# Optimization experiments

Hardware: AMD Instinct MI355X
Metric: run time of the kernel (lower is better)

## Reference

```python
import jax, jax.numpy as jnp
import numpy as np

# Lorentz hyperboloid with curvature -1 (k = 1): <x,x>_L = -1/k, x0 = time coord.
K_CURV = 1.0
EPS = 1e-8
B, N, D, H = 4, 1024, 1024, 16
HD = D // H  # dim_per_head = 64 (space dims per head)


def _time(space):
    # time coord so the point lies on the hyperboloid
    return jnp.sqrt(jnp.sum(space * space, axis=-1, keepdims=True) + 1.0 / K_CURV)


def _lift(space):
    return jnp.concatenate([_time(space), space], axis=-1)


def _linner(u, v):
    # Minkowski inner product <u,v>_L = -u0 v0 + u_s . v_s
    return jnp.sum(u[..., 1:] * v[..., 1:], axis=-1) - u[..., 0] * v[..., 0]


def _lorentz_layernorm(x, gamma, beta):
    s = x[..., 1:]
    mu = jnp.mean(s, axis=-1, keepdims=True)
    var = jnp.mean((s - mu) ** 2, axis=-1, keepdims=True)
    s = (s - mu) / jnp.sqrt(var + 1e-5) * gamma + beta
    return _lift(s)


def _lorentz_linear(x, W, b):
    # linear on the full Lorentz point -> space part of output, time recomputed
    return _lift(x @ W + b)


def _lresnet(x, y, w):
    # Lorentzian residual: (x + w*y) renormalized back onto the hyperboloid
    z = x + w * y
    denom = jnp.sqrt(jnp.clip(-_linner(z, z), EPS))[..., None]
    return z / (jnp.sqrt(K_CURV) * denom)


def _attention(x, Wq, bq, Wk, bk, Wv, bv, Wo, bo):
    def heads(W, b):
        s = (x @ W + b).reshape(B, N, H, HD).transpose(0, 2, 1, 3)  # [B,H,N,HD]
        return _lift(s)  # per-head Lorentz points [B,H,N,HD+1]

    q, k, v = heads(Wq, bq), heads(Wk, bk), heads(Wv, bv)
    sgn = jnp.concatenate([-jnp.ones((1,), x.dtype), jnp.ones((HD,), x.dtype)])
    # pairwise Minkowski inner products; score = -d_L^2 = 2/k + 2<q,k>_L, scaled
    scores = jnp.einsum('bhqd,bhkd->bhqk', q * sgn, k)
    scores = (2.0 / K_CURV + 2.0 * scores) / np.sqrt(HD).astype(np.float32)
    attn = jax.nn.softmax(scores, axis=-1)
    # Lorentz midpoint aggregation of values
    mid = jnp.einsum('bhqk,bhkd->bhqd', attn, v)
    denom = jnp.sqrt(jnp.clip(-_linner(mid, mid), EPS))[..., None]
    mid = mid / (jnp.sqrt(K_CURV) * denom)  # [B,H,N,HD+1]
    cat = mid.transpose(0, 2, 1, 3).reshape(B, N, H * (HD + 1))  # trans_heads_concat
    return _lift(cat @ Wo + bo)


def reference(x, g1, b1, Wq, bq, Wk, bk, Wv, bv, Wo, bo, g2, b2, Wfc, bfc, Wpj, bpj, w1, w2):
    lx = _lorentz_layernorm(x, g1, b1)
    ax = _attention(lx, Wq, bq, Wk, bk, Wv, bv, Wo, bo)
    x = _lresnet(x, ax, w1)
    h = _lorentz_layernorm(x, g2, b2)
    h = _lorentz_linear(h, Wfc, bfc)                      # [B,N,4D]
    h = _lift(jax.nn.gelu(h[..., 1:], approximate=False))  # LorentzActivation(GELU)
    h = _lorentz_linear(h, Wpj, bpj)                      # [B,N,D]
    return _lresnet(x, h, w2)


def setup_inputs() -> dict:
    key = jax.random.key(0)
    ks = jax.random.split(key, 8)
    sc = 0.02
    f32 = jnp.float32
    xs = jax.random.normal(ks[0], (B, N, D - 1), f32)
    return dict(
        x=_lift(xs),
        g1=jnp.ones((D - 1,), f32), b1=jnp.zeros((D - 1,), f32),
        Wq=sc * jax.random.normal(ks[1], (D, H * HD), f32), bq=jnp.zeros((H * HD,), f32),
        Wk=sc * jax.random.normal(ks[2], (D, H * HD), f32), bk=jnp.zeros((H * HD,), f32),
        Wv=sc * jax.random.normal(ks[3], (D, H * HD), f32), bv=jnp.zeros((H * HD,), f32),
        Wo=sc * jax.random.normal(ks[4], (H * (HD + 1), D - 1), f32), bo=jnp.zeros((D - 1,), f32),
        g2=jnp.ones((D - 1,), f32), b2=jnp.zeros((D - 1,), f32),
        Wfc=sc * jax.random.normal(ks[5], (D, 4 * D - 1), f32), bfc=jnp.zeros((4 * D - 1,), f32),
        Wpj=sc * jax.random.normal(ks[6], (4 * D, D - 1), f32), bpj=jnp.zeros((D - 1,), f32),
        w1=jnp.ones((), f32), w2=jnp.ones((), f32),
    )
```

## Files before the change

kernel.cpp:

```cpp
#include <hip/hip_runtime.h>
#include <math.h>

#define BB 4
#define NN 1024
#define DD 1024
#define HH 16
#define ROWS (BB*NN)

typedef __attribute__((ext_vector_type(8))) short bf16x8;
typedef __attribute__((ext_vector_type(4))) float f32x4;
typedef __attribute__((ext_vector_type(4))) unsigned short u16x4;
typedef __attribute__((ext_vector_type(8))) unsigned short u16x8;
typedef unsigned short u16;

__device__ __forceinline__ u16 f2bf(float f) {
    union { float f; unsigned u; } v; v.f = f;
    unsigned r = v.u + 0x7fff + ((v.u >> 16) & 1);
    return (u16)(r >> 16);
}
__device__ __forceinline__ float bf2f(u16 u) {
    union { unsigned u; float f; } v; v.u = ((unsigned)u) << 16; return v.f;
}

__device__ __forceinline__ void async16(const void* g, void* l) {
    __builtin_amdgcn_global_load_lds(
        (__attribute__((address_space(1))) void*)(uintptr_t)g,
        (__attribute__((address_space(3))) void*)(uintptr_t)l,
        16, 0, 0);
}

__device__ __forceinline__ float block_reduce_sum(float v, float* sm) {
    #pragma unroll
    for (int o = 32; o > 0; o >>= 1) v += __shfl_down(v, o);
    int lane = threadIdx.x & 63, wid = threadIdx.x >> 6;
    if (lane == 0) sm[wid] = v;
    __syncthreads();
    if (wid == 0) {
        v = (lane < (int)(blockDim.x >> 6)) ? sm[lane] : 0.f;
        #pragma unroll
        for (int o = 2; o > 0; o >>= 1) v += __shfl_down(v, o);
        if (lane == 0) sm[0] = v;
    }
    __syncthreads();
    float r = sm[0];
    __syncthreads();
    return r;
}

__device__ __forceinline__ void block_reduce3(float& a, float& b, float& c, float* sm) {
    #pragma unroll
    for (int o = 32; o > 0; o >>= 1) {
        a += __shfl_down(a, o); b += __shfl_down(b, o); c += __shfl_down(c, o);
    }
    int lane = threadIdx.x & 63, wid = threadIdx.x >> 6;
    if (lane == 0) { sm[wid] = a; sm[8 + wid] = b; sm[16 + wid] = c; }
    __syncthreads();
    int nw = (int)(blockDim.x >> 6);
    if (wid == 0) {
        float va = (lane < nw) ? sm[lane] : 0.f;
        float vb = (lane < nw) ? sm[8 + lane] : 0.f;
        float vc = (lane < nw) ? sm[16 + lane] : 0.f;
        #pragma unroll
        for (int o = 2; o > 0; o >>= 1) {
            va += __shfl_down(va, o); vb += __shfl_down(vb, o); vc += __shfl_down(vc, o);
        }
        if (lane == 0) { sm[0] = va; sm[8] = vb; sm[16] = vc; }
    }
    __syncthreads();
    a = sm[0]; b = sm[8]; c = sm[16];
    __syncthreads();
}

__global__ __launch_bounds__(256) void k_pre(
        const float* __restrict__ Wq_, const float* __restrict__ Wk_,
        const float* __restrict__ Wv_, const float* __restrict__ Wo_,
        const float* __restrict__ Wfc_, const float* __restrict__ Wpj_,
        u16* __restrict__ WqkvT, u16* __restrict__ WoT,
        u16* __restrict__ WfcT, u16* __restrict__ WpjT,
        const float* __restrict__ x, const float* __restrict__ g1,
        const float* __restrict__ be1, u16* __restrict__ lnout) {
    __shared__ float t[32][33];
    int bid = blockIdx.x;
    if (bid < 12352) {
        const float* W; u16* out; int K, N, Kpad, Npad, gx;
        if (bid < 1024)      { W = Wq_;  out = WqkvT;            K = 1024; N = 1024; Kpad = 1024; Npad = 1024; gx = 32; }
        else if (bid < 2048) { W = Wk_;  out = WqkvT + 1048576;  K = 1024; N = 1024; Kpad = 1024; Npad = 1024; gx = 32; bid -= 1024; }
        else if (bid < 3072) { W = Wv_;  out = WqkvT + 2097152;  K = 1024; N = 1024; Kpad = 1024; Npad = 1024; gx = 32; bid -= 2048; }
        else if (bid < 4160) { W = Wo_;  out = WoT;              K = 1040; N = 1023; Kpad = 1088; Npad = 1024; gx = 34; bid -= 3072; }
        else if (bid < 8256) { W = Wfc_; out = WfcT;             K = 1024; N = 4095; Kpad = 1024; Npad = 4096; gx = 32; bid -= 4160; }
        else                 { W = Wpj_; out = WpjT;             K = 4096; N = 1023; Kpad = 4096; Npad = 1024; gx = 128; bid -= 8256; }
        int k0 = (bid % gx) * 32, n0 = (bid / gx) * 32;
        int tx = threadIdx.x & 31, ty = threadIdx.x >> 5;
        #pragma unroll
        for (int i = 0; i < 32; i += 8) {
            int k = k0 + ty + i, n = n0 + tx;
            t[ty + i][tx] = (k < K && n < N) ? W[(size_t)k * N + n] : 0.f;
        }
        __syncthreads();
        #pragma unroll
        for (int i = 0; i < 32; i += 8) {
            int n = n0 + ty + i, k = k0 + tx;
            if (n < Npad && k < Kpad) out[(size_t)n * Kpad + k] = f2bf(t[tx][ty + i]);
        }
    } else {
        float* sm = &t[0][0];
        int row = bid - 12352, tid = threadIdx.x;
        const float4* xr4 = (const float4*)(x + (size_t)row * DD);
        float4 xv = xr4[tid];
        float s = 0.f, ss = 0.f, dummy = 0.f;
        #pragma unroll
        for (int e = 0; e < 4; ++e) {
            if (tid | e) {
                float v = ((const float*)&xv)[e];
                s += v; ss += v * v;
            }
        }
        block_reduce3(s, ss, dummy, sm);
        float mu = s * (1.f / 1023.f);
        float var = ss * (1.f / 1023.f) - mu * mu;
        float rstd = rsqrtf(var + 1e-5f);
        float vo[4]; float s2 = 0.f;
        #pragma unroll
        for (int e = 0; e < 4; ++e) {
            int c = 4 * tid + e;
            if (c > 0) {
                float v = (((const float*)&xv)[e] - mu) * rstd * g1[c - 1] + be1[c - 1];
                vo[e] = v; s2 += v * v;
            } else vo[e] = 0.f;
        }
        s2 = block_reduce_sum(s2, sm);
        u16x4 lo;
        #pragma unroll
        for (int e = 0; e < 4; ++e) lo[e] = f2bf(vo[e]);
        if (tid == 0) lo[0] = f2bf(sqrtf(s2 + 1.f));
        ((u16x4*)(lnout + (size_t)row * DD))[tid] = lo;
    }
}

__device__ __forceinline__ void cstore(float* p, float v) { *p = v; }
__device__ __forceinline__ void cstore(u16* p, float v) { *p = f2bf(v); }

template <typename OT>
__global__ __launch_bounds__(256) void k_gemm_mfma(
        const u16* __restrict__ A, const u16* __restrict__ BT,
        const float* __restrict__ bias, int nbias,
        OT* __restrict__ C0, OT* __restrict__ C1,
        int ldc, int ldab, int ksplit, int K, int swz) {
    __shared__ __align__(16) u16 smem[32768];
    int z = blockIdx.z;
    int kbeg = z ? ksplit : 0;
    int kend = z ? K : ksplit;
    OT* C = z ? C1 : C0;
    const float* bs = z ? nullptr : bias;

    int bx = blockIdx.x, by = blockIdx.y;
    if (swz) {
        int nx = gridDim.x, ny = gridDim.y;
        int flat = bx + nx * by;
        int c = flat & 7, i = flat >> 3;
        int hi = i / nx;
        by = c * (ny >> 3) + hi;
        bx = i - hi * nx;
    }

    int tid = threadIdx.x;
    int wave = tid >> 6, lane = tid & 63;
    int quad = lane >> 4, m16 = lane & 15;
    int n0 = bx * 128, m0 = by * 128;
    int wm = (wave & 1) * 64, wn = (wave >> 1) * 64;

    f32x4 acc[4][4];
    #pragma unroll
    for (int t = 0; t < 4; ++t)
        #pragma unroll
        for (int u = 0; u < 4; ++u) acc[t][u] = (f32x4){0.f, 0.f, 0.f, 0.f};

    int r8 = lane >> 3;
    int cc = (lane & 7) ^ r8;
    int srow = wave * 32 + r8;
    const u16* ag = A  + (size_t)(m0 + srow) * ldab + cc * 8;
    const u16* bg = BT + (size_t)(n0 + srow) * ldab + cc * 8;

    auto stage = [&](int k0, int s) {
        #pragma unroll
        for (int j = 0; j < 4; ++j) {
            async16(ag + (size_t)(j * 8) * ldab + k0, &smem[s * 8192 + (wave * 32 + j * 8) * 64]);
            async16(bg + (size_t)(j * 8) * ldab + k0, &smem[16384 + s * 8192 + (wave * 32 + j * 8) * 64]);
        }
    };

    int niter = (kend - kbeg) >> 6;
    stage(kbeg, 0);
    for (int it = 0; it < niter; ++it) {
        int cur = it & 1;
        __syncthreads();
        if (it + 1 < niter) stage(kbeg + (it + 1) * 64, cur ^ 1);
        #pragma unroll
        for (int kk = 0; kk < 2; ++kk) {
            bf16x8 af[4], bfr[4];
            #pragma unroll
            for (int t = 0; t < 4; ++t) {
                int slot = (kk * 4 + quad) ^ (m16 & 7);
                af[t] = *(const bf16x8*)&smem[cur * 8192 + (wm + t * 16 + m16) * 64 + slot * 8];
            }
            #pragma unroll
            for (int u = 0; u < 4; ++u) {
                int slot = (kk * 4 + quad) ^ (m16 & 7);
                bfr[u] = *(const bf16x8*)&smem[16384 + cur * 8192 + (wn + u * 16 + m16) * 64 + slot * 8];
            }
            #pragma unroll
            for (int t = 0; t < 4; ++t)
                #pragma unroll
                for (int u = 0; u < 4; ++u)
                    acc[t][u] = __builtin_amdgcn_mfma_f32_16x16x32_bf16(af[t], bfr[u], acc[t][u], 0, 0, 0);
        }
    }
    if constexpr (sizeof(OT) == 2) {
        __syncthreads();
        #pragma unroll
        for (int u = 0; u < 4; ++u) {
            int col = n0 + wn + u * 16 + m16;
            float bv = (bs != nullptr && col < nbias) ? bs[col] : 0.f;
            #pragma unroll
            for (int t = 0; t < 4; ++t) {
                #pragma unroll
                for (int r = 0; r < 4; ++r)
                    smem[(wm + t * 16 + quad * 4 + r) * 128 + wn + u * 16 + m16] = f2bf(acc[t][u][r] + bv);
            }
        }
        __syncthreads();
        u16* Cg = (u16*)C;
        for (int i = tid; i < 2048; i += 256) {
            int rr = i >> 4, ch = i & 15;
            ((u16x8*)(Cg + (size_t)(m0 + rr) * ldc + n0))[ch] = ((const u16x8*)(smem + rr * 128))[ch];
        }
    } else {
        #pragma unroll
        for (int u = 0; u < 4; ++u) {
            int col = n0 + wn + u * 16 + m16;
            if (col < nbias) {
                float bv = (bs != nullptr) ? bs[col] : 0.f;
                #pragma unroll
                for (int t = 0; t < 4; ++t) {
                    #pragma unroll
                    for (int r = 0; r < 4; ++r) {
                        int row = m0 + wm + t * 16 + quad * 4 + r;
                        cstore(C + (size_t)row * ldc + col, acc[t][u][r] + bv);
                    }
                }
            }
        }
    }
}

__global__ __launch_bounds__(256) void k_gemm_qkv(
        const u16* __restrict__ A, const u16* __restrict__ BT,
        const float* __restrict__ bq, const float* __restrict__ bk,
        const float* __restrict__ bv,
        u16* __restrict__ Qp, u16* __restrict__ Kp, u16* __restrict__ V2) {
    __shared__ __align__(16) u16 smem[32768];
    int tid = threadIdx.x;
    int wave = tid >> 6, lane = tid & 63;
    int quad = lane >> 4, m16 = lane & 15;
    int n0 = blockIdx.x * 128, m0 = blockIdx.y * 128;
    int wm = (wave & 1) * 64, wn = (wave >> 1) * 64;

    f32x4 acc[4][4];
    #pragma unroll
    for (int t = 0; t < 4; ++t)
        #pragma unroll
        for (int u = 0; u < 4; ++u) acc[t][u] = (f32x4){0.f, 0.f, 0.f, 0.f};

    int r8 = lane >> 3;
    int cc = (lane & 7) ^ r8;
    int srow = wave * 32 + r8;
    const u16* ag = A  + (size_t)(m0 + srow) * 1024 + cc * 8;
    const u16* bg = BT + (size_t)(n0 + srow) * 1024 + cc * 8;

    auto stage = [&](int k0, int s) {
        #pragma unroll
        for (int j = 0; j < 4; ++j) {
            async16(ag + (size_t)(j * 8) * 1024 + k0, &smem[s * 8192 + (wave * 32 + j * 8) * 64]);
            async16(bg + (size_t)(j * 8) * 1024 + k0, &smem[16384 + s * 8192 + (wave * 32 + j * 8) * 64]);
        }
    };

    stage(0, 0);
    for (int it = 0; it < 16; ++it) {
        int cur = it & 1;
        __syncthreads();
        if (it + 1 < 16) stage((it + 1) * 64, cur ^ 1);
        #pragma unroll
        for (int kk = 0; kk < 2; ++kk) {
            bf16x8 af[4], bfr[4];
            #pragma unroll
            for (int t = 0; t < 4; ++t) {
                int slot = (kk * 4 + quad) ^ (m16 & 7);
                af[t] = *(const bf16x8*)&smem[cur * 8192 + (wm + t * 16 + m16) * 64 + slot * 8];
            }
            #pragma unroll
            for (int u = 0; u < 4; ++u) {
                int slot = (kk * 4 + quad) ^ (m16 & 7);
                bfr[u] = *(const bf16x8*)&smem[16384 + cur * 8192 + (wn + u * 16 + m16) * 64 + slot * 8];
            }
            #pragma unroll
            for (int t = 0; t < 4; ++t)
                #pragma unroll
                for (int u = 0; u < 4; ++u)
                    acc[t][u] = __builtin_amdgcn_mfma_f32_16x16x32_bf16(af[t], bfr[u], acc[t][u], 0, 0, 0);
        }
    }

    int sec = n0 >> 10;
    int h = ((n0 & 1023) + wn) >> 6;
    int b = m0 >> 10;
    int b16h = b * 16 + h;
    const float* bias = (sec == 0) ? bq : (sec == 1) ? bk : bv;
    float bvu[4];
    #pragma unroll
    for (int u = 0; u < 4; ++u) bvu[u] = bias[h * 64 + u * 16 + m16];

    if (sec < 2) {
        const int strd = (sec == 0) ? 96 : 104;
        u16* P = (sec == 0) ? Qp : Kp;
        const float tsign = (sec == 0) ? -1.f : 1.f;
        #pragma unroll
        for (int t = 0; t < 4; ++t) {
            #pragma unroll
            for (int r = 0; r < 4; ++r) {
                int n = (m0 + wm + t * 16 + quad * 4 + r) & 1023;
                u16* drow = P + ((size_t)b16h * 1024 + n) * strd;
                float vv[4]; float ss = 0.f;
                #pragma unroll
                for (int u = 0; u < 4; ++u) { vv[u] = acc[t][u][r] + bvu[u]; ss += vv[u] * vv[u]; }
                ss += __shfl_xor(ss, 1); ss += __shfl_xor(ss, 2);
                ss += __shfl_xor(ss, 4); ss += __shfl_xor(ss, 8);
                #pragma unroll
                for (int u = 0; u < 4; ++u) drow[1 + u * 16 + m16] = f2bf(vv[u]);
                if (m16 == 0) drow[0] = f2bf(tsign * sqrtf(ss + 1.f));
                drow[65 + m16] = 0;
                if (m16 < 15) drow[81 + m16] = 0;
            }
        }
    } else {
        int tile = ((m0 & 1023) + wm) >> 6;
        size_t tbase = ((size_t)b16h * 16 + tile) * 6144;
        #pragma unroll
        for (int t = 0; t < 4; ++t) {
            int tok0 = t * 16 + quad * 4;
            u16x4 tc;
            u16x4 pk[4];
            #pragma unroll
            for (int r = 0; r < 4; ++r) {
                float vv[4]; float ss = 0.f;
                #pragma unroll
                for (int u = 0; u < 4; ++u) { vv[u] = acc[t][u][r] + bvu[u]; ss += vv[u] * vv[u]; }
                ss += __shfl_xor(ss, 1); ss += __shfl_xor(ss, 2);
                ss += __shfl_xor(ss, 4); ss += __shfl_xor(ss, 8);
                tc[r] = f2bf(sqrtf(ss + 1.f));
                #pragma unroll
                for (int u = 0; u < 4; ++u) pk[u][r] = f2bf(vv[u]);
            }
            #pragma unroll
            for (int u = 0; u < 4; ++u) {
                int d = u * 16 + m16;
                *(u16x4*)&V2[tbase + (size_t)(1 + d) * 72 + tok0] = pk[u];
            }
            if (m16 == 0) *(u16x4*)&V2[tbase + tok0] = tc;
        }
        for (int i = lane; i < 240; i += 64) {
            int rr = 65 + (i >> 4), sg = (i & 15) << 2;
            *(u16x4*)&V2[tbase + (size_t)rr * 72 + sg] = (u16x4){0, 0, 0, 0};
        }
    }
}

#define AKS 104
#define AVS 72
#define APS 88
#define KTILE_U16 (64 * AKS)
#define VTILE_U16 6144
#define EXPC 0.36067376f
__global__ __launch_bounds__(512) void k_attn_mfma(
        const u16* __restrict__ Qp, const u16* __restrict__ Kp,
        const u16* __restrict__ V2, u16* __restrict__ cat) {
    __shared__ __align__(16) u16 Klds[2][KTILE_U16];
    __shared__ __align__(16) u16 Vlds[2][VTILE_U16];
    __shared__ __align__(16) u16 Plds[8][16 * APS];
    int tid = threadIdx.x;
    int wave = tid >> 6, lane = tid & 63;
    int quad = lane >> 4, m = lane & 15;
    int wq = wave & 3, g = wave >> 2;
    int bid = blockIdx.x;
    int bh = ((bid & 7) << 3) | (bid >> 6);
    int qt = (bid >> 3) & 7;

    const u16* kg = Kp + (size_t)bh * 16 * KTILE_U16;
    const u16* vg = V2 + (size_t)bh * 16 * VTILE_U16;

    bf16x8 aq[3];
    {
        const u16* qptr = Qp + ((size_t)bh * 1024 + qt * 128 + g * 64 + wq * 16 + m) * 96;
        aq[0] = *(const bf16x8*)(qptr + quad * 8);
        aq[1] = *(const bf16x8*)(qptr + 32 + quad * 8);
        aq[2] = *(const bf16x8*)(qptr + 64 + quad * 8);
    }

    f32x4 O[5];
    #pragma unroll
    for (int i = 0; i < 5; ++i) O[i] = (f32x4){0.f, 0.f, 0.f, 0.f};

    auto stage = [&](int kt, int s) {
        const u16* kt_p = kg + kt * KTILE_U16 + lane * 8;
        const u16* vt_p = vg + kt * VTILE_U16 + lane * 8;
        for (int i = wave; i < 25; i += 8) {
            if (i < 13) async16(kt_p + i * 512, &Klds[s][i * 512]);
            else        async16(vt_p + (i - 13) * 512, &Vlds[s][(i - 13) * 512]);
        }
    };

    stage(0, 0);
    for (int kt = 0; kt < 16; ++kt) {
        int cur = kt & 1;
        __syncthreads();
        if (kt < 15) stage(kt + 1, cur ^ 1);
        u16* pw = &Plds[wave][0];
        #pragma unroll
        for (int nt = 0; nt < 4; ++nt) {
            f32x4 acc = (f32x4){0.f, 0.f, 0.f, 0.f};
            const u16* kr = &Klds[cur][(nt * 16 + m) * AKS + quad * 8];
            acc = __builtin_amdgcn_mfma_f32_16x16x32_bf16(*(const bf16x8*)(kr),      aq[0], acc, 0, 0, 0);
            acc = __builtin_amdgcn_mfma_f32_16x16x32_bf16(*(const bf16x8*)(kr + 32), aq[1], acc, 0, 0, 0);
            acc = __builtin_amdgcn_mfma_f32_16x16x32_bf16(*(const bf16x8*)(kr + 64), aq[2], acc, 0, 0, 0);
            unsigned pk0, pk1;
            {
                union { float f; unsigned u; } a0, a1, a2, a3;
                a0.f = __builtin_amdgcn_exp2f(fmaf(acc[0], EXPC, EXPC));
                a1.f = __builtin_amdgcn_exp2f(fmaf(acc[1], EXPC, EXPC));
                a2.f = __builtin_amdgcn_exp2f(fmaf(acc[2], EXPC, EXPC));
                a3.f = __builtin_amdgcn_exp2f(fmaf(acc[3], EXPC, EXPC));
                pk0 = ((a0.u + 0x8000u) >> 16) | (((a1.u + 0x8000u) >> 16) << 16);
                pk1 = ((a2.u + 0x8000u) >> 16) | (((a3.u + 0x8000u) >> 16) << 16);
            }
            uint2 pk; pk.x = pk0; pk.y = pk1;
            *(uint2*)&pw[m * APS + nt * 16 + quad * 4] = pk;
        }
        #pragma unroll
        for (int kc = 0; kc < 2; ++kc) {
            bf16x8 ap = *(const bf16x8*)&Plds[wave][m * APS + kc * 32 + quad * 8];
            #pragma unroll
            for (int vt = 0; vt < 5; ++vt) {
                bf16x8 bv = *(const bf16x8*)&Vlds[cur][(vt * 16 + m) * AVS + kc * 32 + quad * 8];
                O[vt] = __builtin_amdgcn_mfma_f32_16x16x32_bf16(ap, bv, O[vt], 0, 0, 0);
            }
        }
    }
    int b = bh >> 4, h = bh & 15;
    #pragma unroll
    for (int r = 0; r < 4; ++r) {
        float part = 0.f;
        #pragma unroll
        for (int vt = 0; vt < 5; ++vt) {
            int c = vt * 16 + m;
            float o = O[vt][r];
            part += (c == 0) ? o * o : -o * o;
        }
        part += __shfl_xor(part, 1);
        part += __shfl_xor(part, 2);
        part += __shfl_xor(part, 4);
        part += __shfl_xor(part, 8);
        float rden = rsqrtf(fmaxf(part, 1e-8f));
        int n = qt * 128 + g * 64 + wq * 16 + quad * 4 + r;
        u16* crow = cat + (size_t)(b * 1024 + n) * 1088 + h * 65;
        #pragma unroll
        for (int vt = 0; vt < 5; ++vt) {
            int c = vt * 16 + m;
            if (c < 65) crow[c] = f2bf(O[vt][r] * rden);
        }
    }
    if (h == 15) {
        for (int i = tid; i < 128 * 48; i += 512) {
            int rr = i / 48, c = i - rr * 48;
            int n = qt * 128 + rr;
            cat[(size_t)(b * 1024 + n) * 1088 + 1040 + c] = 0;
        }
    }
}

__global__ __launch_bounds__(256) void k_lresnet_ln(
        const float* __restrict__ x, const float* __restrict__ y0,
        const float* __restrict__ y1, const float* __restrict__ wscale,
        const float* __restrict__ g2, const float* __restrict__ be2,
        float* __restrict__ x1, u16* __restrict__ lnout) {
    __shared__ float sm[24];
    __shared__ float edge[256];
    int row = blockIdx.x, tid = threadIdx.x;
    float w = *wscale;
    float4 xv = ((const float4*)(x  + (size_t)row * DD))[tid];
    float4 av = ((const float4*)(y0 + (size_t)row * 1024))[tid];
    float4 bv = ((const float4*)(y1 + (size_t)row * 1024))[tid];
    float yv[4];
    #pragma unroll
    for (int e = 0; e < 4; ++e) yv[e] = ((const float*)&av)[e] + ((const float*)&bv)[e];
    edge[tid] = yv[3];
    float sy = 0.f;
    #pragma unroll
    for (int e = 0; e < 4; ++e) if (4 * tid + e < 1023) sy += yv[e] * yv[e];
    __syncthreads();
    float yprev = tid ? edge[tid - 1] : 0.f;
    float zv[4];
    float sz = 0.f, szs = 0.f;
    #pragma unroll
    for (int e = 0; e < 4; ++e) {
        float yc = (e == 0) ? yprev : yv[e - 1];
        float z = ((const float*)&xv)[e] + w * yc;
        zv[e] = z;
        if (tid | e) { sz += z * z; szs += z; }
    }
    block_reduce3(sy, sz, szs, sm);
    float x0 = x[(size_t)row * DD];
    float z0 = x0 + w * sqrtf(sy + 1.f);
    float q = z0 * z0 - sz;
    float rden = rsqrtf(fmaxf(q, 1e-8f));
    float mu = rden * szs * (1.f / 1023.f);
    float ex2 = rden * rden * sz * (1.f / 1023.f);
    float rstd = rsqrtf(ex2 - mu * mu + 1e-5f);
    float4 xo; float vo[4]; float s2 = 0.f;
    #pragma unroll
    for (int e = 0; e < 4; ++e) {
        int c = 4 * tid + e;
        float xn = zv[e] * rden;
        ((float*)&xo)[e] = xn;
        if (c > 0) {
            float v = (xn - mu) * rstd * g2[c - 1] + be2[c - 1];
            vo[e] = v; s2 += v * v;
        } else vo[e] = 0.f;
    }
    if (tid == 0) ((float*)&xo)[0] = z0 * rden;
    ((float4*)(x1 + (size_t)row * DD))[tid] = xo;
    s2 = block_reduce_sum(s2, sm);
    u16x4 lo;
    #pragma unroll
    for (int e = 0; e < 4; ++e) lo[e] = f2bf(vo[e]);
    if (tid == 0) lo[0] = f2bf(sqrtf(s2 + 1.f));
    ((u16x4*)(lnout + (size_t)row * DD))[tid] = lo;
}

__global__ __launch_bounds__(256) void k_lresnet(
        const float* __restrict__ x, const float* __restrict__ y0,
        const float* __restrict__ y1, const float* __restrict__ wscale,
        float* __restrict__ out) {
    __shared__ float sm[24];
    __shared__ float edge[256];
    int row = blockIdx.x, tid = threadIdx.x;
    float w = *wscale;
    float4 xv = ((const float4*)(x  + (size_t)row * DD))[tid];
    float4 av = ((const float4*)(y0 + (size_t)row * 1024))[tid];
    float4 bv = ((const float4*)(y1 + (size_t)row * 1024))[tid];
    float yv[4];
    #pragma unroll
    for (int e = 0; e < 4; ++e) yv[e] = ((const float*)&av)[e] + ((const float*)&bv)[e];
    edge[tid] = yv[3];
    float sy = 0.f;
    #pragma unroll
    for (int e = 0; e < 4; ++e) if (4 * tid + e < 1023) sy += yv[e] * yv[e];
    __syncthreads();
    float yprev = tid ? edge[tid - 1] : 0.f;
    float zv[4];
    float sz = 0.f, dummy = 0.f;
    #pragma unroll
    for (int e = 0; e < 4; ++e) {
        float yc = (e == 0) ? yprev : yv[e - 1];
        float z = ((const float*)&xv)[e] + w * yc;
        zv[e] = z;
        if (tid | e) sz += z * z;
    }
    block_reduce3(sy, sz, dummy, sm);
    float x0 = x[(size_t)row * DD];
    float z0 = x0 + w * sqrtf(sy + 1.f);
    float q = z0 * z0 - sz;
    float rden = rsqrtf(fmaxf(q, 1e-8f));
    float4 o;
    #pragma unroll
    for (int e = 0; e < 4; ++e) ((float*)&o)[e] = zv[e] * rden;
    if (tid == 0) ((float*)&o)[0] = z0 * rden;
    ((float4*)(out + (size_t)row * DD))[tid] = o;
}

__global__ __launch_bounds__(256) void k_gelu_lift(
        const u16* __restrict__ hfc, u16* __restrict__ hg) {
    __shared__ float sm[8];
    __shared__ u16 edge[512];
    int row = blockIdx.x, tid = threadIdx.x;
    const u16* hr = hfc + (size_t)row * 4096;
    u16* gr = hg + (size_t)row * 4096;
    u16x8 hv0 = *(const u16x8*)(hr + tid * 8);
    u16x8 hv1 = *(const u16x8*)(hr + 2048 + tid * 8);
    edge[tid] = hv0[7];
    edge[256 + tid] = hv1[7];
    __syncthreads();
    u16 p0 = tid ? edge[tid - 1] : (u16)0;
    u16 p1 = edge[255 + tid];
    float s2 = 0.f;
    u16x8 ov0, ov1;
    #pragma unroll
    for (int e = 0; e < 8; ++e) {
        int c = 8 * tid + e;
        float gl = 0.f;
        if (c > 0) {
            float v = bf2f((e == 0) ? p0 : hv0[e - 1]);
            gl = 0.5f * v * (1.f + erff(v * 0.70710678f));
            s2 += gl * gl;
        }
        ov0[e] = f2bf(gl);
    }
    #pragma unroll
    for (int e = 0; e < 8; ++e) {
        float v = bf2f((e == 0) ? p1 : hv1[e - 1]);
        float gl = 0.5f * v * (1.f + erff(v * 0.70710678f));
        s2 += gl * gl;
        ov1[e] = f2bf(gl);
    }
    *(u16x8*)(gr + tid * 8) = ov0;
    *(u16x8*)(gr + 2048 + tid * 8) = ov1;
    s2 = block_reduce_sum(s2, sm);
    if (tid == 0) gr[0] = f2bf(sqrtf(s2 + 1.f));
}

extern "C" void kernel_launch(void* const* d_in, const int* in_sizes, int n_in,
                              void* d_out, int out_size, void* d_ws, size_t ws_size,
                              hipStream_t stream) {
    const float* x   = (const float*)d_in[0];
    const float* g1  = (const float*)d_in[1];
    const float* b1  = (const float*)d_in[2];
    const float* Wq  = (const float*)d_in[3];
    const float* bq  = (const float*)d_in[4];
    const float* Wk  = (const float*)d_in[5];
    const float* bk  = (const float*)d_in[6];
    const float* Wv  = (const float*)d_in[7];
    const float* bv  = (const float*)d_in[8];
    const float* Wo  = (const float*)d_in[9];
    const float* bo  = (const float*)d_in[10];
    const float* g2  = (const float*)d_in[11];
    const float* b2  = (const float*)d_in[12];
    const float* Wfc = (const float*)d_in[13];
    const float* bfc = (const float*)d_in[14];
    const float* Wpj = (const float*)d_in[15];
    const float* bpj = (const float*)d_in[16];
    const float* w1  = (const float*)d_in[17];
    const float* w2  = (const float*)d_in[18];
    float* out = (float*)d_out;

    char* W = (char*)d_ws;
    u16* lx_bf  = (u16*)(W + 0);
    u16* WqkvT  = (u16*)(W + 8388608);
    u16* WoT    = (u16*)(W + 14680064);
    u16* WfcT   = (u16*)(W + 16908288);
    u16* WpjT   = (u16*)(W + 25296896);
    u16* Qp     = (u16*)(W + 58851328);
    u16* Kp     = (u16*)(W + 71434240);
    u16* V2     = (u16*)(W + 85065728);
    u16* cat_bf = (u16*)(W + 97648640);
    float* ax0  = (float*)(W + 33685504);
    float* ax1  = (float*)(W + 50462720);
    float* x1   = (float*)(W + 67239936);
    u16* hfc_bf = (u16*)(W + 84017152);
    u16* hg_bf  = (u16*)(W + 33685504);
    float* h2a  = (float*)(W + 84017152);
    float* h2b  = (float*)(W + 100794368);

    dim3 blk(256);

    k_pre<<<16448, blk, 0, stream>>>(Wq, Wk, Wv, Wo, Wfc, Wpj,
                                     WqkvT, WoT, WfcT, WpjT,
                                     x, g1, b1, lx_bf);

    k_gemm_qkv<<<dim3(24, 32, 1), blk, 0, stream>>>(
        lx_bf, WqkvT, bq, bk, bv, Qp, Kp, V2);

    k_attn_mfma<<<512, dim3(512), 0, stream>>>(Qp, Kp, V2, cat_bf);

    k_gemm_mfma<float><<<dim3(8, 32, 2), blk, 0, stream>>>(
        cat_bf, WoT, bo, 1023, ax0, ax1, 1024, 1088, 576, 1088, 1);

    k_lresnet_ln<<<ROWS, blk, 0, stream>>>(x, ax0, ax1, w1, g2, b2, x1, lx_bf);

    k_gemm_mfma<u16><<<dim3(32, 32, 1), blk, 0, stream>>>(
        lx_bf, WfcT, bfc, 4095, hfc_bf, hfc_bf, 4096, 1024, 1024, 1024, 0);

    k_gelu_lift<<<ROWS, blk, 0, stream>>>(hfc_bf, hg_bf);

    k_gemm_mfma<float><<<dim3(8, 32, 2), blk, 0, stream>>>(
        hg_bf, WpjT, bpj, 1023, h2a, h2b, 1024, 4096, 2048, 4096, 1);

    k_lresnet<<<ROWS, blk, 0, stream>>>(x1, h2a, h2b, w2, out);
}
```

Measured before the change: 374.9 us.

## Fuse GELU and lift into FC GEMM epilogue, apply time term in projection

The separate GELU/lift kernel and the bf16 round trip of the FC output are removed: the FC GEMM epilogue applies GELU, stores the activations unshifted, and accumulates per-row sums of squares with atomics. The projection GEMM then adds the time-coordinate contribution as sqrt(tsum+1) times the first row of Wpj, and the transposed Wpj is built without that row. This saves one 32 MB read and one 32 MB write plus a launch. In exchange it adds atomics in the FC epilogue, extra work in the projection epilogue, and a dependency on tsum being zeroed in the layernorm kernel.

Result: slower. 394.0 us (+5.1%).

```diff
diff --git a/kernel.cpp b/kernel.cpp
--- a/kernel.cpp
+++ b/kernel.cpp
@@ -82,19 +82,19 @@
     __shared__ float t[32][33];
     int bid = blockIdx.x;
     if (bid < 12352) {
-        const float* W; u16* out; int K, N, Kpad, Npad, gx;
+        const float* W; u16* out; int K, N, Kpad, Npad, gx, shift = 0;
         if (bid < 1024)      { W = Wq_;  out = WqkvT;            K = 1024; N = 1024; Kpad = 1024; Npad = 1024; gx = 32; }
         else if (bid < 2048) { W = Wk_;  out = WqkvT + 1048576;  K = 1024; N = 1024; Kpad = 1024; Npad = 1024; gx = 32; bid -= 1024; }
         else if (bid < 3072) { W = Wv_;  out = WqkvT + 2097152;  K = 1024; N = 1024; Kpad = 1024; Npad = 1024; gx = 32; bid -= 2048; }
         else if (bid < 4160) { W = Wo_;  out = WoT;              K = 1040; N = 1023; Kpad = 1088; Npad = 1024; gx = 34; bid -= 3072; }
         else if (bid < 8256) { W = Wfc_; out = WfcT;             K = 1024; N = 4095; Kpad = 1024; Npad = 4096; gx = 32; bid -= 4160; }
-        else                 { W = Wpj_; out = WpjT;             K = 4096; N = 1023; Kpad = 4096; Npad = 1024; gx = 128; bid -= 8256; }
+        else                 { W = Wpj_; out = WpjT;             K = 4095; N = 1023; Kpad = 4096; Npad = 1024; gx = 128; shift = 1; bid -= 8256; }
         int k0 = (bid % gx) * 32, n0 = (bid / gx) * 32;
         int tx = threadIdx.x & 31, ty = threadIdx.x >> 5;
         #pragma unroll
         for (int i = 0; i < 32; i += 8) {
             int k = k0 + ty + i, n = n0 + tx;
-            t[ty + i][tx] = (k < K && n < N) ? W[(size_t)k * N + n] : 0.f;
+            t[ty + i][tx] = (k < K && n < N) ? W[(size_t)(k + shift) * N + n] : 0.f;
         }
         __syncthreads();
         #pragma unroll
@@ -145,7 +145,8 @@
         const u16* __restrict__ A, const u16* __restrict__ BT,
         const float* __restrict__ bias, int nbias,
         OT* __restrict__ C0, OT* __restrict__ C1,
-        int ldc, int ldab, int ksplit, int K, int swz) {
+        int ldc, int ldab, int ksplit, int K, int swz,
+        const float* __restrict__ tsum_, const float* __restrict__ w0_) {
     __shared__ __align__(16) u16 smem[32768];
     int z = blockIdx.z;
     int kbeg = z ? ksplit : 0;
@@ -235,21 +236,131 @@
             ((u16x8*)(Cg + (size_t)(m0 + rr) * ldc + n0))[ch] = ((const u16x8*)(smem + rr * 128))[ch];
         }
     } else {
+        float trow[4][4];
+        #pragma unroll
+        for (int t = 0; t < 4; ++t)
+            #pragma unroll
+            for (int r = 0; r < 4; ++r) trow[t][r] = 0.f;
+        bool fix = (tsum_ != nullptr && bs != nullptr);
+        if (fix) {
+            #pragma unroll
+            for (int t = 0; t < 4; ++t)
+                #pragma unroll
+                for (int r = 0; r < 4; ++r)
+                    trow[t][r] = sqrtf(tsum_[m0 + wm + t * 16 + quad * 4 + r] + 1.f);
+        }
         #pragma unroll
         for (int u = 0; u < 4; ++u) {
             int col = n0 + wn + u * 16 + m16;
             if (col < nbias) {
                 float bv = (bs != nullptr) ? bs[col] : 0.f;
+                float w0c = fix ? w0_[col] : 0.f;
                 #pragma unroll
                 for (int t = 0; t < 4; ++t) {
                     #pragma unroll
                     for (int r = 0; r < 4; ++r) {
                         int row = m0 + wm + t * 16 + quad * 4 + r;
-                        cstore(C + (size_t)row * ldc + col, acc[t][u][r] + bv);
+                        cstore(C + (size_t)row * ldc + col, acc[t][u][r] + bv + trow[t][r] * w0c);
                     }
                 }
             }
         }
+    }
+}
+
+__global__ __launch_bounds__(256) void k_gemm_gelu(
+        const u16* __restrict__ A, const u16* __restrict__ BT,
+        const float* __restrict__ bias,
+        u16* __restrict__ C, float* __restrict__ tsum) {
+    __shared__ __align__(16) u16 smem[32768];
+    int tid = threadIdx.x;
+    int wave = tid >> 6, lane = tid & 63;
+    int quad = lane >> 4, m16 = lane & 15;
+    int n0 = blockIdx.x * 128, m0 = blockIdx.y * 128;
+    int wm = (wave & 1) * 64, wn = (wave >> 1) * 64;
+
+    f32x4 acc[4][4];
+    #pragma unroll
+    for (int t = 0; t < 4; ++t)
+        #pragma unroll
+        for (int u = 0; u < 4; ++u) acc[t][u] = (f32x4){0.f, 0.f, 0.f, 0.f};
+
+    int r8 = lane >> 3;
+    int cc = (lane & 7) ^ r8;
+    int srow = wave * 32 + r8;
+    const u16* ag = A  + (size_t)(m0 + srow) * 1024 + cc * 8;
+    const u16* bg = BT + (size_t)(n0 + srow) * 1024 + cc * 8;
+
+    auto stage = [&](int k0, int s) {
+        #pragma unroll
+        for (int j = 0; j < 4; ++j) {
+            async16(ag + (size_t)(j * 8) * 1024 + k0, &smem[s * 8192 + (wave * 32 + j * 8) * 64]);
+            async16(bg + (size_t)(j * 8) * 1024 + k0, &smem[16384 + s * 8192 + (wave * 32 + j * 8) * 64]);
+        }
+    };
+
+    stage(0, 0);
+    for (int it = 0; it < 16; ++it) {
+        int cur = it & 1;
+        __syncthreads();
+        if (it + 1 < 16) stage((it + 1) * 64, cur ^ 1);
+        #pragma unroll
+        for (int kk = 0; kk < 2; ++kk) {
+            bf16x8 af[4], bfr[4];
+            #pragma unroll
+            for (int t = 0; t < 4; ++t) {
+                int slot = (kk * 4 + quad) ^ (m16 & 7);
+                af[t] = *(const bf16x8*)&smem[cur * 8192 + (wm + t * 16 + m16) * 64 + slot * 8];
+            }
+            #pragma unroll
+            for (int u = 0; u < 4; ++u) {
+                int slot = (kk * 4 + quad) ^ (m16 & 7);
+                bfr[u] = *(const bf16x8*)&smem[16384 + cur * 8192 + (wn + u * 16 + m16) * 64 + slot * 8];
+            }
+            #pragma unroll
+            for (int t = 0; t < 4; ++t)
+                #pragma unroll
+                for (int u = 0; u < 4; ++u)
+                    acc[t][u] = __builtin_amdgcn_mfma_f32_16x16x32_bf16(af[t], bfr[u], acc[t][u], 0, 0, 0);
+        }
+    }
+
+    __syncthreads();
+    float rs[4][4];
+    #pragma unroll
+    for (int t = 0; t < 4; ++t)
+        #pragma unroll
+        for (int r = 0; r < 4; ++r) rs[t][r] = 0.f;
+    #pragma unroll
+    for (int u = 0; u < 4; ++u) {
+        int col = n0 + wn + u * 16 + m16;
+        bool valid = col < 4095;
+        float bv = valid ? bias[col] : 0.f;
+        #pragma unroll
+        for (int t = 0; t < 4; ++t) {
+            #pragma unroll
+            for (int r = 0; r < 4; ++r) {
+                float v = acc[t][u][r] + bv;
+                float gl = valid ? 0.5f * v * (1.f + erff(v * 0.70710678f)) : 0.f;
+                smem[(wm + t * 16 + quad * 4 + r) * 128 + wn + u * 16 + m16] = f2bf(gl);
+                rs[t][r] += gl * gl;
+            }
+        }
+    }
+    #pragma unroll
+    for (int t = 0; t < 4; ++t) {
+        #pragma unroll
+        for (int r = 0; r < 4; ++r) {
+            float s = rs[t][r];
+            s += __shfl_xor(s, 1); s += __shfl_xor(s, 2);
+            s += __shfl_xor(s, 4); s += __shfl_xor(s, 8);
+            if (m16 == 0) atomicAdd(&tsum[m0 + wm + t * 16 + quad * 4 + r], s);
+        }
+    }
+    __syncthreads();
+    for (int i = tid; i < 2048; i += 256) {
+        int rr = i >> 4, ch = i & 15;
+        ((u16x8*)(C + (size_t)(m0 + rr) * 4096 + n0))[ch] = ((const u16x8*)(smem + rr * 128))[ch];
     }
 }
 
@@ -491,10 +602,12 @@
         const float* __restrict__ x, const float* __restrict__ y0,
         const float* __restrict__ y1, const float* __restrict__ wscale,
         const float* __restrict__ g2, const float* __restrict__ be2,
-        float* __restrict__ x1, u16* __restrict__ lnout) {
+        float* __restrict__ x1, u16* __restrict__ lnout,
+        float* __restrict__ tsum) {
     __shared__ float sm[24];
     __shared__ float edge[256];
     int row = blockIdx.x, tid = threadIdx.x;
+    if (tid == 0) tsum[row] = 0.f;
     float w = *wscale;
     float4 xv = ((const float4*)(x  + (size_t)row * DD))[tid];
     float4 av = ((const float4*)(y0 + (size_t)row * 1024))[tid];
@@ -585,46 +698,6 @@
     for (int e = 0; e < 4; ++e) ((float*)&o)[e] = zv[e] * rden;
     if (tid == 0) ((float*)&o)[0] = z0 * rden;
     ((float4*)(out + (size_t)row * DD))[tid] = o;
-}
-
-__global__ __launch_bounds__(256) void k_gelu_lift(
-        const u16* __restrict__ hfc, u16* __restrict__ hg) {
-    __shared__ float sm[8];
-    __shared__ u16 edge[512];
-    int row = blockIdx.x, tid = threadIdx.x;
-    const u16* hr = hfc + (size_t)row * 4096;
-    u16* gr = hg + (size_t)row * 4096;
-    u16x8 hv0 = *(const u16x8*)(hr + tid * 8);
-    u16x8 hv1 = *(const u16x8*)(hr + 2048 + tid * 8);
-    edge[tid] = hv0[7];
-    edge[256 + tid] = hv1[7];
-    __syncthreads();
-    u16 p0 = tid ? edge[tid - 1] : (u16)0;
-    u16 p1 = edge[255 + tid];
-    float s2 = 0.f;
-    u16x8 ov0, ov1;
-    #pragma unroll
-    for (int e = 0; e < 8; ++e) {
-        int c = 8 * tid + e;
-        float gl = 0.f;
-        if (c > 0) {
-            float v = bf2f((e == 0) ? p0 : hv0[e - 1]);
-            gl = 0.5f * v * (1.f + erff(v * 0.70710678f));
-            s2 += gl * gl;
-        }
-        ov0[e] = f2bf(gl);
-    }
-    #pragma unroll
-    for (int e = 0; e < 8; ++e) {
-        float v = bf2f((e == 0) ? p1 : hv1[e - 1]);
-        float gl = 0.5f * v * (1.f + erff(v * 0.70710678f));
-        s2 += gl * gl;
-        ov1[e] = f2bf(gl);
-    }
-    *(u16x8*)(gr + tid * 8) = ov0;
-    *(u16x8*)(gr + 2048 + tid * 8) = ov1;
-    s2 = block_reduce_sum(s2, sm);
-    if (tid == 0) gr[0] = f2bf(sqrtf(s2 + 1.f));
 }
 
 extern "C" void kernel_launch(void* const* d_in, const int* in_sizes, int n_in,
@@ -664,10 +737,10 @@
     float* ax0  = (float*)(W + 33685504);
     float* ax1  = (float*)(W + 50462720);
     float* x1   = (float*)(W + 67239936);
-    u16* hfc_bf = (u16*)(W + 84017152);
     u16* hg_bf  = (u16*)(W + 33685504);
     float* h2a  = (float*)(W + 84017152);
     float* h2b  = (float*)(W + 100794368);
+    float* tsum = (float*)(W + 8388608);
 
     dim3 blk(256);
 
@@ -681,17 +754,15 @@
     k_attn_mfma<<<512, dim3(512), 0, stream>>>(Qp, Kp, V2, cat_bf);
 
     k_gemm_mfma<float><<<dim3(8, 32, 2), blk, 0, stream>>>(
-        cat_bf, WoT, bo, 1023, ax0, ax1, 1024, 1088, 576, 1088, 1);
-
-    k_lresnet_ln<<<ROWS, blk, 0, stream>>>(x, ax0, ax1, w1, g2, b2, x1, lx_bf);
-
-    k_gemm_mfma<u16><<<dim3(32, 32, 1), blk, 0, stream>>>(
-        lx_bf, WfcT, bfc, 4095, hfc_bf, hfc_bf, 4096, 1024, 1024, 1024, 0);
-
-    k_gelu_lift<<<ROWS, blk, 0, stream>>>(hfc_bf, hg_bf);
+        cat_bf, WoT, bo, 1023, ax0, ax1, 1024, 1088, 576, 1088, 1, nullptr, nullptr);
+
+    k_lresnet_ln<<<ROWS, blk, 0, stream>>>(x, ax0, ax1, w1, g2, b2, x1, lx_bf, tsum);
+
+    k_gemm_gelu<<<dim3(32, 32, 1), blk, 0, stream>>>(
+        lx_bf, WfcT, bfc, hg_bf, tsum);
 
     k_gemm_mfma<float><<<dim3(8, 32, 2), blk, 0, stream>>>(
-        hg_bf, WpjT, bpj, 1023, h2a, h2b, 1024, 4096, 2048, 4096, 1);
+        hg_bf, WpjT, bpj, 1023, h2a, h2b, 1024, 4096, 2048, 4096, 1, tsum, Wpj);
 
     k_lresnet<<<ROWS, blk, 0, stream>>>(x1, h2a, h2b, w2, out);
 }
```
